# Kernel optimization log

Measured on AMD Instinct MI355X. Metric: run time of the kernel, lower is better.

Reference implementation:

```python
import jax, jax.numpy as jnp
import numpy as np

B, L, D, H = 2, 2048, 2048, 16
HD = D // H


def _rope_tables(max_len, dim):
    # pair i uses freq 10000^{-2i/dim}; values repeated for the (even, odd) slots
    inv_freq = 1.0 / (10000.0 ** (np.arange(0, dim, 2, dtype=np.float32) / dim))
    ang = np.arange(max_len, dtype=np.float32)[:, None] * inv_freq[None, :]  # [L, dim/2]
    cos = np.repeat(np.cos(ang), 2, axis=-1)  # [L, dim]
    sin = np.repeat(np.sin(ang), 2, axis=-1)
    return jnp.asarray(cos), jnp.asarray(sin)


def setup_inputs() -> dict:
    key = jax.random.key(0)
    k1, k2, k3 = jax.random.split(key, 3)
    x = jax.random.normal(k1, (B, L, D), dtype=jnp.float32)
    cos, sin = _rope_tables(L, D)
    bound = np.sqrt(6.0 / ((1 + 2.236**2) * D))  # kaiming_uniform_ a=2.236
    Wqkv = jax.random.uniform(k2, (3 * D, D), jnp.float32, -bound, bound)
    Wo = jax.random.uniform(k3, (D, D), jnp.float32, -bound, bound)
    return {"x": x, "cos": cos, "sin": sin, "Wqkv": Wqkv, "Wo": Wo}


def _rotate_emb(x, cos, sin):
    # x: [B, L, D]; interleaved rotation over full model dim, as in source
    x1, x2 = x[..., ::2], x[..., 1::2]
    x_rot = jnp.stack((-x2, x1), axis=-1).reshape(x.shape)
    Lx = x.shape[1]
    return x * cos[:Lx] + x_rot * sin[:Lx]


def reference(x, cos, sin, Wqkv, Wo):
    qkv = jnp.einsum('bld,ed->ble', x, Wqkv)  # [B, L, 3D]
    q, k, v = jnp.split(qkv, 3, axis=-1)
    q = _rotate_emb(q, cos, sin)
    k = _rotate_emb(k, cos, sin)
    # [B, H, L, HD]
    q = q.reshape(B, L, H, HD).transpose(0, 2, 1, 3)
    k = k.reshape(B, L, H, HD).transpose(0, 2, 1, 3)
    v = v.reshape(B, L, H, HD).transpose(0, 2, 1, 3)
    scale = 1.0 / np.sqrt(HD)  # SDPA default scale (flash path, mask=None -> causal)
    scores = jnp.einsum('bhqd,bhkd->bhqk', q, k) * scale
    causal = jnp.tril(jnp.ones((L, L), dtype=bool))
    scores = jnp.where(causal, scores, -jnp.inf)
    attn = jax.nn.softmax(scores, axis=-1)
    out = jnp.einsum('bhqk,bhkd->bhqd', attn, v)
    out = out.transpose(0, 2, 1, 3).reshape(B, L, D)
    return jnp.einsum('bld,ed->ble', out, Wo)
```

## Files before the change

kernel.cpp:

```cpp
#include <hip/hip_runtime.h>
#include <cstdint>
#include <cstddef>


typedef __attribute__((ext_vector_type(8))) short s16x8;
typedef __attribute__((ext_vector_type(4))) float f32x4;

__device__ inline unsigned short f2bf(float f) {
  unsigned int u = __builtin_bit_cast(unsigned int, f);
  u = (u + 0x7FFFu + ((u >> 16) & 1u)) >> 16;
  return (unsigned short)u;
}

__device__ inline float bf2f(unsigned short b) {
  unsigned int u = ((unsigned int)b) << 16;
  return __builtin_bit_cast(float, u);
}

__device__ inline void gl_lds16(const void* g, void* l) {
  __builtin_amdgcn_global_load_lds(
      (const __attribute__((address_space(1))) unsigned int*)g,
      (__attribute__((address_space(3))) unsigned int*)l, 16, 0, 0);
}

__global__ __launch_bounds__(256)
void cvt_kernel(const float* __restrict__ in, unsigned short* __restrict__ out,
                int n4) {
  int i = blockIdx.x * 256 + threadIdx.x;
  if (i >= n4) return;
  float4 v = ((const float4*)in)[i];
  ushort4 o;
  o.x = f2bf(v.x); o.y = f2bf(v.y); o.z = f2bf(v.z); o.w = f2bf(v.w);
  ((ushort4*)out)[i] = o;
}

__global__ __launch_bounds__(256, 2)
void gemm_qkv_rope(const unsigned short* __restrict__ A,
                   const unsigned short* __restrict__ Bw,
                   const float* __restrict__ cosT,
                   const float* __restrict__ sinT,
                   unsigned short* __restrict__ qb,
                   unsigned short* __restrict__ kb,
                   unsigned short* __restrict__ vb) {
  __shared__ unsigned short smem[128 * 136];
  unsigned short* lA = smem;
  unsigned short* lB = smem + 4096;
  const int tid = threadIdx.x;
  const int lane = tid & 63, wave = tid >> 6;
  const int quad = lane >> 4, l16 = lane & 15;
  const int wm = wave >> 1, wn = wave & 1;
  const int m0 = blockIdx.y * 128, n0 = blockIdx.x * 128;

  f32x4 acc[4][4];
  for (int i = 0; i < 4; i++)
    for (int j = 0; j < 4; j++) acc[i][j] = (f32x4){0.f, 0.f, 0.f, 0.f};

  const int srow = tid >> 2;
  const int se = (tid & 3) * 8;
  const unsigned short* Ap = A + (size_t)(m0 + srow) * 2048 + se;
  const unsigned short* Bp = Bw + (size_t)(n0 + srow) * 2048 + se;

  for (int k0 = 0; k0 < 2048; k0 += 32) {
    gl_lds16(Ap + k0,                     &lA[tid * 8]);
    gl_lds16(Ap + (size_t)64 * 2048 + k0, &lA[2048 + tid * 8]);
    gl_lds16(Bp + k0,                     &lB[tid * 8]);
    gl_lds16(Bp + (size_t)64 * 2048 + k0, &lB[2048 + tid * 8]);
    __syncthreads();
    s16x8 af[4], bfr[4];
    for (int i = 0; i < 4; i++)
      af[i] = *(const s16x8*)&lA[(wm * 64 + i * 16 + l16) * 32 + quad * 8];
    for (int i = 0; i < 4; i++)
      bfr[i] = *(const s16x8*)&lB[(wn * 64 + i * 16 + l16) * 32 + quad * 8];
    for (int mi = 0; mi < 4; mi++)
      for (int ni = 0; ni < 4; ni++)
        acc[mi][ni] = __builtin_amdgcn_mfma_f32_16x16x32_bf16(
            af[mi], bfr[ni], acc[mi][ni], 0, 0, 0);
    __syncthreads();
  }

  for (int mi = 0; mi < 4; mi++)
    for (int ni = 0; ni < 4; ni++)
      for (int r = 0; r < 4; r++) {
        const int row = wm * 64 + mi * 16 + quad * 4 + r;
        const int col = wn * 64 + ni * 16 + l16;
        smem[row * 136 + col] = f2bf(acc[mi][ni][r]);
      }
  __syncthreads();

  const int section = n0 >> 11;
  const int nnb = n0 & 2047;
  const int h = nnb >> 7;
  unsigned short* dst = (section == 0) ? qb : (section == 1) ? kb : vb;

  for (int i = 0; i < 8; i++) {
    const int chunk = i * 256 + tid;
    const int row = chunk >> 4;
    const int c8 = (chunk & 15) * 8;
    s16x8 vv = *(const s16x8*)&smem[row * 136 + c8];
    float f[8];
    for (int j = 0; j < 8; j++) f[j] = bf2f((unsigned short)vv[j]);
    const int m = m0 + row, b = m >> 11, l = m & 2047;
    if (section < 2) {
      float ca[8], sa[8];
      const size_t tb = (size_t)l * 2048 + nnb + c8;
      *(float4*)&ca[0] = *(const float4*)&cosT[tb];
      *(float4*)&ca[4] = *(const float4*)&cosT[tb + 4];
      *(float4*)&sa[0] = *(const float4*)&sinT[tb];
      *(float4*)&sa[4] = *(const float4*)&sinT[tb + 4];
      float o_[8];
      for (int t = 0; t < 4; t++) {
        o_[2 * t]     = f[2 * t] * ca[2 * t]         - f[2 * t + 1] * sa[2 * t];
        o_[2 * t + 1] = f[2 * t + 1] * ca[2 * t + 1] + f[2 * t] * sa[2 * t + 1];
      }
      for (int j = 0; j < 8; j++) f[j] = o_[j];
    }
    s16x8 ov;
    for (int j = 0; j < 8; j++) ov[j] = (short)f2bf(f[j]);
    *(s16x8*)&dst[((size_t)(b * 16 + h) * 2048 + l) * 128 + c8] = ov;
  }
}

__global__ __launch_bounds__(256)
void transpose_v(const unsigned short* __restrict__ vb,
                 unsigned short* __restrict__ vtb) {
  __shared__ unsigned short t[64 * 136];
  const int kt = blockIdx.x, bh = blockIdx.y;
  const int tid = threadIdx.x;
  const unsigned short* src = vb + ((size_t)bh * 2048 + kt * 64) * 128;
  for (int i = 0; i < 4; i++) {
    const int chunk = i * 256 + tid;
    const int row = chunk >> 4, c8 = (chunk & 15) * 8;
    *(s16x8*)&t[row * 136 + c8] = *(const s16x8*)&src[row * 128 + c8];
  }
  __syncthreads();
  unsigned short* dst = vtb + ((size_t)bh * 32 + kt) * 8192;
  for (int i = 0; i < 4; i++) {
    const int oc = i * 256 + tid;
    const int kk = oc >> 9;
    const int hd = (oc >> 2) & 127;
    const int k8 = (oc & 3) * 8;
    s16x8 v;
    for (int j = 0; j < 8; j++) v[j] = t[(kk * 32 + k8 + j) * 136 + hd];
    *(s16x8*)&dst[oc * 8] = v;
  }
}

__global__ __launch_bounds__(256, 2)
void attn_kernel(const unsigned short* __restrict__ qb,
                 const unsigned short* __restrict__ kb,
                 const unsigned short* __restrict__ vtb,
                 unsigned short* __restrict__ ob) {
  __shared__ unsigned short lK[2][4 * 64 * 32];
  __shared__ unsigned short lV[2][2 * 128 * 32];
  __shared__ unsigned short lP[4 * 16 * 88];
  const int tid = threadIdx.x;
  const int lane = tid & 63, wave = tid >> 6;
  const int quad = lane >> 4, l16 = lane & 15;

  const int id = blockIdx.x;
  const int xcd = id & 7, slot = id >> 3;
  const int bh = xcd * 4 + (slot >> 4);
  const int p = slot & 15;

  const unsigned short* Q = qb + (size_t)bh * 2048 * 128;
  const unsigned short* K = kb + (size_t)bh * 2048 * 128;
  const unsigned short* VT = vtb + (size_t)bh * 32 * 8192;
  const int b = bh >> 4, h = bh & 15;

  unsigned short* P = &lP[wave * 16 * 88];
  const float scale = 0.08838834764831845f;
  const int skey = tid >> 2, se = (tid & 3) * 8;

  for (int phase = 0; phase < 2; phase++) {
    const int qt = phase ? p : (31 - p);
    const int q0 = qt * 64;

    const int qrow = q0 + wave * 16 + l16;
    s16x8 qf[4];
    for (int kk = 0; kk < 4; kk++)
      qf[kk] = *(const s16x8*)&Q[(size_t)qrow * 128 + kk * 32 + quad * 8];

    f32x4 o[8];
    for (int i = 0; i < 8; i++) o[i] = (f32x4){0.f, 0.f, 0.f, 0.f};
    float mrow[4], lrow[4];
    for (int r = 0; r < 4; r++) { mrow[r] = -3.0e38f; lrow[r] = 0.f; }

    {
      const unsigned short* Kt = K + (size_t)skey * 128 + se;
      for (int i = 0; i < 4; i++)
        gl_lds16(Kt + i * 32, &lK[0][i * 2048 + tid * 8]);
      const unsigned short* Vt = VT + tid * 8;
      for (int i = 0; i < 4; i++)
        gl_lds16(Vt + i * 2048, &lV[0][i * 2048 + tid * 8]);
    }

    for (int kt = 0; kt <= qt; kt++) {
      const int buf = kt & 1;
      __syncthreads();
      if (kt < qt) {
        const unsigned short* Kt = K + (size_t)((kt + 1) * 64 + skey) * 128 + se;
        for (int i = 0; i < 4; i++)
          gl_lds16(Kt + i * 32, &lK[buf ^ 1][i * 2048 + tid * 8]);
        const unsigned short* Vt = VT + (size_t)(kt + 1) * 8192 + tid * 8;
        for (int i = 0; i < 4; i++)
          gl_lds16(Vt + i * 2048, &lV[buf ^ 1][i * 2048 + tid * 8]);
      }

      f32x4 s[4];
      for (int i = 0; i < 4; i++) s[i] = (f32x4){0.f, 0.f, 0.f, 0.f};
      for (int kk = 0; kk < 4; kk++)
        for (int ni = 0; ni < 4; ni++) {
          const s16x8 bfr = *(const s16x8*)
              &lK[buf][kk * 2048 + (ni * 16 + l16) * 32 + quad * 8];
          s[ni] = __builtin_amdgcn_mfma_f32_16x16x32_bf16(qf[kk], bfr, s[ni],
                                                          0, 0, 0);
        }

      const bool diag = (kt == qt);
      float alpha[4];
      for (int r = 0; r < 4; r++) {
        float v0 = s[0][r] * scale, v1 = s[1][r] * scale;
        float v2 = s[2][r] * scale, v3 = s[3][r] * scale;
        if (diag) {
          const int qi = q0 + wave * 16 + quad * 4 + r;
          const int j0 = kt * 64 + l16;
          v0 = (j0 > qi) ? -3.0e38f : v0;
          v1 = (j0 + 16 > qi) ? -3.0e38f : v1;
          v2 = (j0 + 32 > qi) ? -3.0e38f : v2;
          v3 = (j0 + 48 > qi) ? -3.0e38f : v3;
        }
        float mx = fmaxf(fmaxf(v0, v1), fmaxf(v2, v3));
        for (int off = 1; off < 16; off <<= 1)
          mx = fmaxf(mx, __shfl_xor(mx, off, 64));
        const float mnew = fmaxf(mrow[r], mx);
        alpha[r] = __expf(mrow[r] - mnew);
        const float p0 = __expf(v0 - mnew), p1 = __expf(v1 - mnew);
        const float p2 = __expf(v2 - mnew), p3 = __expf(v3 - mnew);
        s[0][r] = p0; s[1][r] = p1; s[2][r] = p2; s[3][r] = p3;
        lrow[r] = lrow[r] * alpha[r] + (p0 + p1 + p2 + p3);
        mrow[r] = mnew;
      }
      for (int i = 0; i < 8; i++)
        for (int r = 0; r < 4; r++) o[i][r] *= alpha[r];

      for (int ni = 0; ni < 4; ni++)
        for (int r = 0; r < 4; r++)
          P[(quad * 4 + r) * 88 + ni * 16 + l16] = f2bf(s[ni][r]);

      for (int kk = 0; kk < 2; kk++) {
        const s16x8 pf = *(const s16x8*)&P[l16 * 88 + kk * 32 + quad * 8];
        for (int ni = 0; ni < 8; ni++) {
          const s16x8 vf = *(const s16x8*)
              &lV[buf][kk * 4096 + (ni * 16 + l16) * 32 + quad * 8];
          o[ni] = __builtin_amdgcn_mfma_f32_16x16x32_bf16(pf, vf, o[ni],
                                                          0, 0, 0);
        }
      }
    }

    for (int r = 0; r < 4; r++) {
      float ls = lrow[r];
      for (int off = 1; off < 16; off <<= 1) ls += __shfl_xor(ls, off, 64);
      const float inv = 1.f / ls;
      const int q = q0 + wave * 16 + quad * 4 + r;
      unsigned short* orow = ob + ((size_t)(b * 2048 + q)) * 2048 + h * 128;
      for (int ni = 0; ni < 8; ni++)
        orow[ni * 16 + l16] = f2bf(o[ni][r] * inv);
    }
    __syncthreads();
  }
}

__global__ __launch_bounds__(256, 2)
void gemm_wo(const unsigned short* __restrict__ A,
             const unsigned short* __restrict__ Bw,
             float* __restrict__ out) {
  __shared__ unsigned short lA[128 * 32];
  __shared__ unsigned short lB[128 * 32];
  const int tid = threadIdx.x;
  const int lane = tid & 63, wave = tid >> 6;
  const int quad = lane >> 4, l16 = lane & 15;
  const int wm = wave >> 1, wn = wave & 1;
  const int m0 = blockIdx.y * 128, n0 = blockIdx.x * 128;

  f32x4 acc[4][4];
  for (int i = 0; i < 4; i++)
    for (int j = 0; j < 4; j++) acc[i][j] = (f32x4){0.f, 0.f, 0.f, 0.f};

  const int srow = tid >> 2;
  const int se = (tid & 3) * 8;
  const unsigned short* Ap = A + (size_t)(m0 + srow) * 2048 + se;
  const unsigned short* Bp = Bw + (size_t)(n0 + srow) * 2048 + se;

  for (int k0 = 0; k0 < 2048; k0 += 32) {
    gl_lds16(Ap + k0,                     &lA[tid * 8]);
    gl_lds16(Ap + (size_t)64 * 2048 + k0, &lA[2048 + tid * 8]);
    gl_lds16(Bp + k0,                     &lB[tid * 8]);
    gl_lds16(Bp + (size_t)64 * 2048 + k0, &lB[2048 + tid * 8]);
    __syncthreads();
    s16x8 af[4], bfr[4];
    for (int i = 0; i < 4; i++)
      af[i] = *(const s16x8*)&lA[(wm * 64 + i * 16 + l16) * 32 + quad * 8];
    for (int i = 0; i < 4; i++)
      bfr[i] = *(const s16x8*)&lB[(wn * 64 + i * 16 + l16) * 32 + quad * 8];
    for (int mi = 0; mi < 4; mi++)
      for (int ni = 0; ni < 4; ni++)
        acc[mi][ni] = __builtin_amdgcn_mfma_f32_16x16x32_bf16(
            af[mi], bfr[ni], acc[mi][ni], 0, 0, 0);
    __syncthreads();
  }

  for (int mi = 0; mi < 4; mi++)
    for (int r = 0; r < 4; r++) {
      const int m = m0 + wm * 64 + mi * 16 + quad * 4 + r;
      for (int ni = 0; ni < 4; ni++) {
        const int n = n0 + wn * 64 + ni * 16 + l16;
        out[(size_t)m * 2048 + n] = acc[mi][ni][r];
      }
    }
}

extern "C" void kernel_launch(void* const* d_in, const int* in_sizes, int n_in,
                              void* d_out, int out_size, void* d_ws,
                              size_t ws_size, hipStream_t stream) {
  const float* x    = (const float*)d_in[0];
  const float* cosT = (const float*)d_in[1];
  const float* sinT = (const float*)d_in[2];
  const float* Wqkv = (const float*)d_in[3];
  const float* Wo   = (const float*)d_in[4];
  float* out = (float*)d_out;

  unsigned short* xb    = (unsigned short*)d_ws;
  unsigned short* wqkvb = xb + 8388608;
  unsigned short* wob   = wqkvb + 12582912;
  unsigned short* qb    = wob + 4194304;
  unsigned short* kb    = qb + 8388608;
  unsigned short* vb    = kb + 8388608;
  unsigned short* vtb   = vb + 8388608;
  unsigned short* ob    = vtb + 8388608;

  cvt_kernel<<<8192, 256, 0, stream>>>(x, xb, 2097152);
  cvt_kernel<<<12288, 256, 0, stream>>>(Wqkv, wqkvb, 3145728);
  cvt_kernel<<<4096, 256, 0, stream>>>(Wo, wob, 1048576);

  gemm_qkv_rope<<<dim3(48, 32), 256, 0, stream>>>(xb, wqkvb, cosT, sinT,
                                                  qb, kb, vb);
  transpose_v<<<dim3(32, 32), 256, 0, stream>>>(vb, vtb);
  attn_kernel<<<512, 256, 0, stream>>>(qb, kb, vtb, ob);
  gemm_wo<<<dim3(16, 32), 256, 0, stream>>>(ob, wob, out);
}
```

Measured before the change: 425.1 us.

## Merge conversions, convert rope tables to bf16, fuse V transpose, widen GEMM K-step

After: 383.8 us. 1.11x faster.

```diff
diff --git a/kernel.cpp b/kernel.cpp
--- a/kernel.cpp
+++ b/kernel.cpp
@@ -24,27 +24,40 @@
 }
 
 __global__ __launch_bounds__(256)
-void cvt_kernel(const float* __restrict__ in, unsigned short* __restrict__ out,
-                int n4) {
-  int i = blockIdx.x * 256 + threadIdx.x;
-  if (i >= n4) return;
-  float4 v = ((const float4*)in)[i];
+void cvt_all(const float* __restrict__ x, const float* __restrict__ wqkv,
+             const float* __restrict__ wo, const float* __restrict__ cosT,
+             const float* __restrict__ sinT,
+             unsigned short* __restrict__ xb, unsigned short* __restrict__ wqkvb,
+             unsigned short* __restrict__ wob, unsigned short* __restrict__ cosb,
+             unsigned short* __restrict__ sinb) {
+  const int i = blockIdx.x * 256 + threadIdx.x;
+  const float* src;
+  unsigned short* dst;
+  int off;
+  if (i < 2097152)      { src = x;    dst = xb;    off = i; }
+  else if (i < 5242880) { src = wqkv; dst = wqkvb; off = i - 2097152; }
+  else if (i < 6291456) { src = wo;   dst = wob;   off = i - 5242880; }
+  else if (i < 7340032) { src = cosT; dst = cosb;  off = i - 6291456; }
+  else                  { src = sinT; dst = sinb;  off = i - 7340032; }
+  float4 v = ((const float4*)src)[off];
   ushort4 o;
   o.x = f2bf(v.x); o.y = f2bf(v.y); o.z = f2bf(v.z); o.w = f2bf(v.w);
-  ((ushort4*)out)[i] = o;
+  ((ushort4*)dst)[off] = o;
 }
 
 __global__ __launch_bounds__(256, 2)
 void gemm_qkv_rope(const unsigned short* __restrict__ A,
                    const unsigned short* __restrict__ Bw,
-                   const float* __restrict__ cosT,
-                   const float* __restrict__ sinT,
+                   const unsigned short* __restrict__ cosb,
+                   const unsigned short* __restrict__ sinb,
                    unsigned short* __restrict__ qb,
                    unsigned short* __restrict__ kb,
-                   unsigned short* __restrict__ vb) {
+                   unsigned short* __restrict__ vtb) {
   __shared__ unsigned short smem[128 * 136];
-  unsigned short* lA = smem;
-  unsigned short* lB = smem + 4096;
+  unsigned short* lA0 = smem;
+  unsigned short* lA1 = smem + 4096;
+  unsigned short* lB0 = smem + 8192;
+  unsigned short* lB1 = smem + 12288;
   const int tid = threadIdx.x;
   const int lane = tid & 63, wave = tid >> 6;
   const int quad = lane >> 4, l16 = lane & 15;
@@ -60,21 +73,30 @@
   const unsigned short* Ap = A + (size_t)(m0 + srow) * 2048 + se;
   const unsigned short* Bp = Bw + (size_t)(n0 + srow) * 2048 + se;
 
-  for (int k0 = 0; k0 < 2048; k0 += 32) {
-    gl_lds16(Ap + k0,                     &lA[tid * 8]);
-    gl_lds16(Ap + (size_t)64 * 2048 + k0, &lA[2048 + tid * 8]);
-    gl_lds16(Bp + k0,                     &lB[tid * 8]);
-    gl_lds16(Bp + (size_t)64 * 2048 + k0, &lB[2048 + tid * 8]);
-    __syncthreads();
-    s16x8 af[4], bfr[4];
-    for (int i = 0; i < 4; i++)
-      af[i] = *(const s16x8*)&lA[(wm * 64 + i * 16 + l16) * 32 + quad * 8];
-    for (int i = 0; i < 4; i++)
-      bfr[i] = *(const s16x8*)&lB[(wn * 64 + i * 16 + l16) * 32 + quad * 8];
-    for (int mi = 0; mi < 4; mi++)
-      for (int ni = 0; ni < 4; ni++)
-        acc[mi][ni] = __builtin_amdgcn_mfma_f32_16x16x32_bf16(
-            af[mi], bfr[ni], acc[mi][ni], 0, 0, 0);
+  for (int k0 = 0; k0 < 2048; k0 += 64) {
+    gl_lds16(Ap + k0,                          &lA0[tid * 8]);
+    gl_lds16(Ap + (size_t)64 * 2048 + k0,      &lA0[2048 + tid * 8]);
+    gl_lds16(Ap + k0 + 32,                     &lA1[tid * 8]);
+    gl_lds16(Ap + (size_t)64 * 2048 + k0 + 32, &lA1[2048 + tid * 8]);
+    gl_lds16(Bp + k0,                          &lB0[tid * 8]);
+    gl_lds16(Bp + (size_t)64 * 2048 + k0,      &lB0[2048 + tid * 8]);
+    gl_lds16(Bp + k0 + 32,                     &lB1[tid * 8]);
+    gl_lds16(Bp + (size_t)64 * 2048 + k0 + 32, &lB1[2048 + tid * 8]);
+    __syncthreads();
+#pragma unroll
+    for (int half = 0; half < 2; half++) {
+      const unsigned short* sA = half ? lA1 : lA0;
+      const unsigned short* sB = half ? lB1 : lB0;
+      s16x8 af[4], bfr[4];
+      for (int i = 0; i < 4; i++)
+        af[i] = *(const s16x8*)&sA[(wm * 64 + i * 16 + l16) * 32 + quad * 8];
+      for (int i = 0; i < 4; i++)
+        bfr[i] = *(const s16x8*)&sB[(wn * 64 + i * 16 + l16) * 32 + quad * 8];
+      for (int mi = 0; mi < 4; mi++)
+        for (int ni = 0; ni < 4; ni++)
+          acc[mi][ni] = __builtin_amdgcn_mfma_f32_16x16x32_bf16(
+              af[mi], bfr[ni], acc[mi][ni], 0, 0, 0);
+    }
     __syncthreads();
   }
 
@@ -90,58 +112,49 @@
   const int section = n0 >> 11;
   const int nnb = n0 & 2047;
   const int h = nnb >> 7;
-  unsigned short* dst = (section == 0) ? qb : (section == 1) ? kb : vb;
-
-  for (int i = 0; i < 8; i++) {
-    const int chunk = i * 256 + tid;
-    const int row = chunk >> 4;
-    const int c8 = (chunk & 15) * 8;
-    s16x8 vv = *(const s16x8*)&smem[row * 136 + c8];
-    float f[8];
-    for (int j = 0; j < 8; j++) f[j] = bf2f((unsigned short)vv[j]);
-    const int m = m0 + row, b = m >> 11, l = m & 2047;
-    if (section < 2) {
-      float ca[8], sa[8];
+  const int bblk = m0 >> 11;
+
+  if (section < 2) {
+    unsigned short* dst = (section == 0) ? qb : kb;
+    for (int i = 0; i < 8; i++) {
+      const int chunk = i * 256 + tid;
+      const int row = chunk >> 4;
+      const int c8 = (chunk & 15) * 8;
+      s16x8 vv = *(const s16x8*)&smem[row * 136 + c8];
+      const int l = (m0 & 2047) + row;
       const size_t tb = (size_t)l * 2048 + nnb + c8;
-      *(float4*)&ca[0] = *(const float4*)&cosT[tb];
-      *(float4*)&ca[4] = *(const float4*)&cosT[tb + 4];
-      *(float4*)&sa[0] = *(const float4*)&sinT[tb];
-      *(float4*)&sa[4] = *(const float4*)&sinT[tb + 4];
+      s16x8 cv = *(const s16x8*)&cosb[tb];
+      s16x8 sv = *(const s16x8*)&sinb[tb];
+      float f[8];
+      for (int j = 0; j < 8; j++) f[j] = bf2f((unsigned short)vv[j]);
       float o_[8];
       for (int t = 0; t < 4; t++) {
-        o_[2 * t]     = f[2 * t] * ca[2 * t]         - f[2 * t + 1] * sa[2 * t];
-        o_[2 * t + 1] = f[2 * t + 1] * ca[2 * t + 1] + f[2 * t] * sa[2 * t + 1];
-      }
-      for (int j = 0; j < 8; j++) f[j] = o_[j];
-    }
-    s16x8 ov;
-    for (int j = 0; j < 8; j++) ov[j] = (short)f2bf(f[j]);
-    *(s16x8*)&dst[((size_t)(b * 16 + h) * 2048 + l) * 128 + c8] = ov;
-  }
-}
-
-__global__ __launch_bounds__(256)
-void transpose_v(const unsigned short* __restrict__ vb,
-                 unsigned short* __restrict__ vtb) {
-  __shared__ unsigned short t[64 * 136];
-  const int kt = blockIdx.x, bh = blockIdx.y;
-  const int tid = threadIdx.x;
-  const unsigned short* src = vb + ((size_t)bh * 2048 + kt * 64) * 128;
-  for (int i = 0; i < 4; i++) {
-    const int chunk = i * 256 + tid;
-    const int row = chunk >> 4, c8 = (chunk & 15) * 8;
-    *(s16x8*)&t[row * 136 + c8] = *(const s16x8*)&src[row * 128 + c8];
-  }
-  __syncthreads();
-  unsigned short* dst = vtb + ((size_t)bh * 32 + kt) * 8192;
-  for (int i = 0; i < 4; i++) {
-    const int oc = i * 256 + tid;
-    const int kk = oc >> 9;
-    const int hd = (oc >> 2) & 127;
-    const int k8 = (oc & 3) * 8;
-    s16x8 v;
-    for (int j = 0; j < 8; j++) v[j] = t[(kk * 32 + k8 + j) * 136 + hd];
-    *(s16x8*)&dst[oc * 8] = v;
+        const float c0 = bf2f((unsigned short)cv[2 * t]);
+        const float c1 = bf2f((unsigned short)cv[2 * t + 1]);
+        const float s0 = bf2f((unsigned short)sv[2 * t]);
+        const float s1 = bf2f((unsigned short)sv[2 * t + 1]);
+        o_[2 * t]     = f[2 * t] * c0     - f[2 * t + 1] * s0;
+        o_[2 * t + 1] = f[2 * t + 1] * c1 + f[2 * t] * s1;
+      }
+      s16x8 ov;
+      for (int j = 0; j < 8; j++) ov[j] = (short)f2bf(o_[j]);
+      *(s16x8*)&dst[((size_t)(bblk * 16 + h) * 2048 + l) * 128 + c8] = ov;
+    }
+  } else {
+    const int ktbase = (m0 & 2047) >> 6;
+    const size_t bh32 = ((size_t)(bblk * 16 + h)) * 32;
+    for (int i = 0; i < 8; i++) {
+      const int oc = i * 256 + tid;
+      const int ktl = oc >> 10;
+      const int kk2 = (oc >> 9) & 1;
+      const int hd = (oc >> 2) & 127;
+      const int k8 = (oc & 3) * 8;
+      s16x8 v;
+      for (int j = 0; j < 8; j++)
+        v[j] = smem[(ktl * 64 + kk2 * 32 + k8 + j) * 136 + hd];
+      unsigned short* dv = vtb + (bh32 + ktbase + ktl) * 8192;
+      *(s16x8*)&dv[(kk2 * 128 + hd) * 32 + k8] = v;
+    }
   }
 }
 
@@ -275,8 +288,11 @@
 void gemm_wo(const unsigned short* __restrict__ A,
              const unsigned short* __restrict__ Bw,
              float* __restrict__ out) {
-  __shared__ unsigned short lA[128 * 32];
-  __shared__ unsigned short lB[128 * 32];
+  __shared__ unsigned short smem[4 * 4096];
+  unsigned short* lA0 = smem;
+  unsigned short* lA1 = smem + 4096;
+  unsigned short* lB0 = smem + 8192;
+  unsigned short* lB1 = smem + 12288;
   const int tid = threadIdx.x;
   const int lane = tid & 63, wave = tid >> 6;
   const int quad = lane >> 4, l16 = lane & 15;
@@ -292,21 +308,30 @@
   const unsigned short* Ap = A + (size_t)(m0 + srow) * 2048 + se;
   const unsigned short* Bp = Bw + (size_t)(n0 + srow) * 2048 + se;
 
-  for (int k0 = 0; k0 < 2048; k0 += 32) {
-    gl_lds16(Ap + k0,                     &lA[tid * 8]);
-    gl_lds16(Ap + (size_t)64 * 2048 + k0, &lA[2048 + tid * 8]);
-    gl_lds16(Bp + k0,                     &lB[tid * 8]);
-    gl_lds16(Bp + (size_t)64 * 2048 + k0, &lB[2048 + tid * 8]);
-    __syncthreads();
-    s16x8 af[4], bfr[4];
-    for (int i = 0; i < 4; i++)
-      af[i] = *(const s16x8*)&lA[(wm * 64 + i * 16 + l16) * 32 + quad * 8];
-    for (int i = 0; i < 4; i++)
-      bfr[i] = *(const s16x8*)&lB[(wn * 64 + i * 16 + l16) * 32 + quad * 8];
-    for (int mi = 0; mi < 4; mi++)
-      for (int ni = 0; ni < 4; ni++)
-        acc[mi][ni] = __builtin_amdgcn_mfma_f32_16x16x32_bf16(
-            af[mi], bfr[ni], acc[mi][ni], 0, 0, 0);
+  for (int k0 = 0; k0 < 2048; k0 += 64) {
+    gl_lds16(Ap + k0,                          &lA0[tid * 8]);
+    gl_lds16(Ap + (size_t)64 * 2048 + k0,      &lA0[2048 + tid * 8]);
+    gl_lds16(Ap + k0 + 32,                     &lA1[tid * 8]);
+    gl_lds16(Ap + (size_t)64 * 2048 + k0 + 32, &lA1[2048 + tid * 8]);
+    gl_lds16(Bp + k0,                          &lB0[tid * 8]);
+    gl_lds16(Bp + (size_t)64 * 2048 + k0,      &lB0[2048 + tid * 8]);
+    gl_lds16(Bp + k0 + 32,                     &lB1[tid * 8]);
+    gl_lds16(Bp + (size_t)64 * 2048 + k0 + 32, &lB1[2048 + tid * 8]);
+    __syncthreads();
+#pragma unroll
+    for (int half = 0; half < 2; half++) {
+      const unsigned short* sA = half ? lA1 : lA0;
+      const unsigned short* sB = half ? lB1 : lB0;
+      s16x8 af[4], bfr[4];
+      for (int i = 0; i < 4; i++)
+        af[i] = *(const s16x8*)&sA[(wm * 64 + i * 16 + l16) * 32 + quad * 8];
+      for (int i = 0; i < 4; i++)
+        bfr[i] = *(const s16x8*)&sB[(wn * 64 + i * 16 + l16) * 32 + quad * 8];
+      for (int mi = 0; mi < 4; mi++)
+        for (int ni = 0; ni < 4; ni++)
+          acc[mi][ni] = __builtin_amdgcn_mfma_f32_16x16x32_bf16(
+              af[mi], bfr[ni], acc[mi][ni], 0, 0, 0);
+    }
     __syncthreads();
   }
 
@@ -333,19 +358,17 @@
   unsigned short* xb    = (unsigned short*)d_ws;
   unsigned short* wqkvb = xb + 8388608;
   unsigned short* wob   = wqkvb + 12582912;
-  unsigned short* qb    = wob + 4194304;
+  unsigned short* cosb  = wob + 4194304;
+  unsigned short* sinb  = cosb + 4194304;
+  unsigned short* qb    = sinb + 4194304;
   unsigned short* kb    = qb + 8388608;
-  unsigned short* vb    = kb + 8388608;
-  unsigned short* vtb   = vb + 8388608;
+  unsigned short* vtb   = kb + 8388608;
   unsigned short* ob    = vtb + 8388608;
 
-  cvt_kernel<<<8192, 256, 0, stream>>>(x, xb, 2097152);
-  cvt_kernel<<<12288, 256, 0, stream>>>(Wqkv, wqkvb, 3145728);
-  cvt_kernel<<<4096, 256, 0, stream>>>(Wo, wob, 1048576);
-
-  gemm_qkv_rope<<<dim3(48, 32), 256, 0, stream>>>(xb, wqkvb, cosT, sinT,
-                                                  qb, kb, vb);
-  transpose_v<<<dim3(32, 32), 256, 0, stream>>>(vb, vtb);
+  cvt_all<<<32768, 256, 0, stream>>>(x, Wqkv, Wo, cosT, sinT,
+                                     xb, wqkvb, wob, cosb, sinb);
+  gemm_qkv_rope<<<dim3(48, 32), 256, 0, stream>>>(xb, wqkvb, cosb, sinb,
+                                                  qb, kb, vtb);
   attn_kernel<<<512, 256, 0, stream>>>(qb, kb, vtb, ob);
   gemm_wo<<<dim3(16, 32), 256, 0, stream>>>(ob, wob, out);
 }
```
